# Kernel tuning notes

Hardware: AMD Instinct MI355X
Metric: run time of the kernel (lower is better)

Reference implementation:

```python
import jax, jax.numpy as jnp
import numpy as np

D_MODEL = 1024
N_HEADS = 16
D_K = D_MODEL // N_HEADS
B, T = 4, 2048


def setup_inputs() -> dict:
    key = jax.random.key(0)
    ks = jax.random.split(key, 12)
    s = 1.0 / np.sqrt(D_MODEL)
    inp = {
        "query": jax.random.normal(ks[0], (B, T, D_MODEL), dtype=jnp.float32),
        "key": jax.random.normal(ks[1], (B, T, D_MODEL), dtype=jnp.float32),
        "value": jax.random.normal(ks[2], (B, T, D_MODEL), dtype=jnp.float32),
        # causal mask, broadcastable over batch and heads
        "mask": jnp.tril(jnp.ones((T, T), dtype=bool))[None, None, :, :],
        "W_q": jax.random.uniform(ks[3], (D_MODEL, D_MODEL), jnp.float32, -s, s),
        "b_q": jnp.zeros((D_MODEL,), jnp.float32),
        "W_k": jax.random.uniform(ks[4], (D_MODEL, D_MODEL), jnp.float32, -s, s),
        "b_k": jnp.zeros((D_MODEL,), jnp.float32),
        "W_v": jax.random.uniform(ks[5], (D_MODEL, D_MODEL), jnp.float32, -s, s),
        "b_v": jnp.zeros((D_MODEL,), jnp.float32),
        "W_o": jax.random.uniform(ks[6], (D_MODEL, D_MODEL), jnp.float32, -s, s),
        "b_o": jnp.zeros((D_MODEL,), jnp.float32),
    }
    return inp


def _split_heads(x):
    b, t, _ = x.shape
    return x.reshape(b, t, N_HEADS, D_K).transpose(0, 2, 1, 3)  # [B,H,T,Dk]


def reference(query, key, value, mask, W_q, b_q, W_k, b_k, W_v, b_v, W_o, b_o):
    q = _split_heads(query @ W_q.T + b_q)
    k = _split_heads(key @ W_k.T + b_k)
    v = _split_heads(value @ W_v.T + b_v)
    scale = 1.0 / jnp.sqrt(jnp.asarray(D_K, q.dtype))
    scores = jnp.einsum("bhqd,bhkd->bhqk", q, k) * scale  # [B,H,Tq,Tk]
    scores = jnp.where(mask, scores, jnp.asarray(-jnp.inf, scores.dtype))
    attn = jax.nn.softmax(scores, axis=-1)
    out = jnp.einsum("bhqk,bhkd->bhqd", attn, v)
    out = out.transpose(0, 2, 1, 3).reshape(query.shape[0], query.shape[1], D_MODEL)
    return out @ W_o.T + b_o
```

## Files before the change

### kernel.cpp

```cpp
#include <hip/hip_runtime.h>
#include <stdint.h>
#include <stddef.h>


typedef __attribute__((ext_vector_type(4))) float f32x4;
typedef __attribute__((ext_vector_type(8))) _Float16 f16x8;
typedef __attribute__((ext_vector_type(4))) _Float16 f16x4;

#define DEV __device__ __forceinline__

constexpr int BATCH = 4, SEQ = 2048, NH = 16, DK = 64, DM = 1024;
constexpr int MROWS = BATCH * SEQ;
constexpr float QSCALE = 0.125f * 1.4426950408889634f;

DEV void async16(const void* g, void* l) {
  __builtin_amdgcn_global_load_lds(
      (const __attribute__((address_space(1))) unsigned int*)g,
      (__attribute__((address_space(3))) unsigned int*)l, 16, 0, 0);
}

__global__ void cvt_w_kernel(const float* __restrict__ w0, const float* __restrict__ w1,
                             const float* __restrict__ w2, const float* __restrict__ w3,
                             _Float16* __restrict__ o0, _Float16* __restrict__ o1,
                             _Float16* __restrict__ o2, _Float16* __restrict__ o3) {
  size_t i = (size_t)blockIdx.x * blockDim.x + threadIdx.x;
  const float* ws[4] = {w0, w1, w2, w3};
  _Float16* os[4] = {o0, o1, o2, o3};
#pragma unroll
  for (int m = 0; m < 4; m++) {
    f32x4 x = *(const f32x4*)(ws[m] + i * 4);
    f16x4 h;
#pragma unroll
    for (int j = 0; j < 4; j++) h[j] = (_Float16)x[j];
    *(f16x4*)(os[m] + i * 4) = h;
  }
}

__global__ void cvt_act_kernel(const float* __restrict__ a0, const float* __restrict__ a1,
                               const float* __restrict__ a2, _Float16* __restrict__ o0,
                               _Float16* __restrict__ o1, _Float16* __restrict__ o2) {
  size_t i = (size_t)blockIdx.x * blockDim.x + threadIdx.x;
  const float* as[3] = {a0, a1, a2};
  _Float16* os[3] = {o0, o1, o2};
#pragma unroll
  for (int m = 0; m < 3; m++) {
    f32x4 x = *(const f32x4*)(as[m] + i * 4);
    f16x4 h;
#pragma unroll
    for (int j = 0; j < 4; j++) h[j] = (_Float16)x[j];
    *(f16x4*)(os[m] + i * 4) = h;
  }
}

struct QKVPtrs {
  const float* a32[3];
  const _Float16* a16[3];
  const _Float16* w[3];
  const float* bias[3];
  _Float16* out[3];
};

template <bool AH>
__global__ __launch_bounds__(256) void gemm_qkv_kernel(QKVPtrs P) {
  constexpr int K = DM;
  __shared__ __align__(16) _Float16 smem[128 * 144];
  _Float16* As = smem;
  _Float16* Bs = smem + 8192;
  const int z = blockIdx.z;
  const _Float16* Bw = P.w[z];
  const int tid = threadIdx.x;
  const int wave = tid >> 6, lane = tid & 63;
  const int quad = lane >> 4, l16 = lane & 15;
  const int wm = wave >> 1, wn = wave & 1;
  const int m0 = blockIdx.x * 128, n0 = blockIdx.y * 128;
  const float scale = (z == 0) ? QSCALE : 1.0f;

  const f32x4 zero4 = {0.f, 0.f, 0.f, 0.f};
  f32x4 acc[4][4];
#pragma unroll
  for (int mt = 0; mt < 4; mt++)
#pragma unroll
    for (int nt = 0; nt < 4; nt++) acc[mt][nt] = zero4;

  float bv[4];
#pragma unroll
  for (int nt = 0; nt < 4; nt++) bv[nt] = P.bias[z][n0 + wn * 64 + nt * 16 + l16];

  for (int kt = 0; kt < K / 64; kt++) {
    const int k0 = kt * 64;
#pragma unroll
    for (int it = 0; it < 4; it++) {
      int idx = it * 256 + tid;
      async16(Bw + (size_t)(n0 + (idx >> 3)) * K + k0 + (idx & 7) * 8,
              (char*)Bs + (size_t)(it * 256 + wave * 64) * 16);
    }
    if (AH) {
      const _Float16* Af = P.a16[z];
#pragma unroll
      for (int it = 0; it < 4; it++) {
        int idx = it * 256 + tid;
        async16(Af + (size_t)(m0 + (idx >> 3)) * K + k0 + (idx & 7) * 8,
                (char*)As + (size_t)(it * 256 + wave * 64) * 16);
      }
    } else {
      const float* Af = P.a32[z];
#pragma unroll
      for (int it = 0; it < 4; it++) {
        int idx = it * 256 + tid;
        int row = idx >> 3, seg = idx & 7;
        const float* g = Af + (size_t)(m0 + row) * K + k0 + seg * 8;
        f32x4 x0 = *(const f32x4*)g;
        f32x4 x1 = *(const f32x4*)(g + 4);
        f16x8 h;
#pragma unroll
        for (int j = 0; j < 4; j++) { h[j] = (_Float16)x0[j]; h[4 + j] = (_Float16)x1[j]; }
        *(f16x8*)&As[row * 64 + seg * 8] = h;
      }
    }
    __syncthreads();
#pragma unroll
    for (int ks = 0; ks < 2; ks++) {
      f16x8 af[4], bfr[4];
#pragma unroll
      for (int mt = 0; mt < 4; mt++)
        af[mt] = *(const f16x8*)&As[(wm * 64 + mt * 16 + l16) * 64 + ks * 32 + quad * 8];
#pragma unroll
      for (int nt = 0; nt < 4; nt++)
        bfr[nt] = *(const f16x8*)&Bs[(wn * 64 + nt * 16 + l16) * 64 + ks * 32 + quad * 8];
#pragma unroll
      for (int mt = 0; mt < 4; mt++)
#pragma unroll
        for (int nt = 0; nt < 4; nt++)
          acc[mt][nt] = __builtin_amdgcn_mfma_f32_16x16x32_f16(af[mt], bfr[nt], acc[mt][nt], 0, 0, 0);
    }
    __syncthreads();
  }

  _Float16* Ct = smem;
  const int b = m0 >> 11, tbase = m0 & (SEQ - 1);
  if (z < 2) {
#pragma unroll
    for (int mt = 0; mt < 4; mt++)
#pragma unroll
      for (int nt = 0; nt < 4; nt++)
#pragma unroll
        for (int i = 0; i < 4; i++)
          Ct[(wm * 64 + mt * 16 + quad * 4 + i) * 144 + wn * 64 + nt * 16 + l16] =
              (_Float16)((acc[mt][nt][i] + bv[nt]) * scale);
  } else {
#pragma unroll
    for (int mt = 0; mt < 4; mt++)
#pragma unroll
      for (int nt = 0; nt < 4; nt++)
#pragma unroll
        for (int i = 0; i < 4; i++)
          Ct[(wn * 64 + nt * 16 + l16) * 144 + wm * 64 + mt * 16 + quad * 4 + i] =
              (_Float16)(acc[mt][nt][i] + bv[nt]);
  }
  __syncthreads();
  _Float16* out = P.out[z];
  if (z < 2) {
    const int row = tid >> 1, coff = (tid & 1) * 32;
#pragma unroll
    for (int hh = 0; hh < 2; hh++) {
      int h = (n0 >> 6) + hh;
      size_t gb = ((size_t)(b * NH + h) * SEQ + tbase) * 64 + (size_t)tid * 32;
#pragma unroll
      for (int k2 = 0; k2 < 4; k2++)
        *(f16x8*)&out[gb + k2 * 8] =
            *(const f16x8*)&Ct[row * 144 + hh * 64 + coff + k2 * 8];
    }
  } else {
#pragma unroll
    for (int k2 = 0; k2 < 8; k2++) {
      int c = k2 * 256 + tid;
      int n = c >> 4, s2 = c & 15;
      int h = (n0 + n) >> 6, d = (n0 + n) & (DK - 1);
      size_t gb = ((size_t)(b * NH + h) * DK + d) * SEQ + tbase + s2 * 8;
      *(f16x8*)&out[gb] = *(const f16x8*)&Ct[n * 144 + s2 * 8];
    }
  }
}

__global__ __launch_bounds__(256) void gemm_out_kernel(
    const _Float16* __restrict__ Ah, const _Float16* __restrict__ Bw,
    const float* __restrict__ bias, float* __restrict__ Cp) {
  constexpr int K = DM;
  __shared__ __align__(16) _Float16 As[128 * 64];
  __shared__ __align__(16) _Float16 Bs[128 * 64];
  const int tid = threadIdx.x;
  const int wave = tid >> 6, lane = tid & 63;
  const int quad = lane >> 4, l16 = lane & 15;
  const int wm = wave >> 1, wn = wave & 1;
  const int m0 = blockIdx.x * 128, n0 = blockIdx.y * 128;

  const f32x4 zero4 = {0.f, 0.f, 0.f, 0.f};
  f32x4 acc[4][4];
#pragma unroll
  for (int mt = 0; mt < 4; mt++)
#pragma unroll
    for (int nt = 0; nt < 4; nt++) acc[mt][nt] = zero4;

  float bv[4];
#pragma unroll
  for (int nt = 0; nt < 4; nt++) bv[nt] = bias[n0 + wn * 64 + nt * 16 + l16];

  for (int kt = 0; kt < K / 64; kt++) {
    const int k0 = kt * 64;
#pragma unroll
    for (int it = 0; it < 4; it++) {
      int idx = it * 256 + tid;
      async16(Bw + (size_t)(n0 + (idx >> 3)) * K + k0 + (idx & 7) * 8,
              (char*)Bs + (size_t)(it * 256 + wave * 64) * 16);
    }
#pragma unroll
    for (int it = 0; it < 4; it++) {
      int idx = it * 256 + tid;
      async16(Ah + (size_t)(m0 + (idx >> 3)) * K + k0 + (idx & 7) * 8,
              (char*)As + (size_t)(it * 256 + wave * 64) * 16);
    }
    __syncthreads();
#pragma unroll
    for (int ks = 0; ks < 2; ks++) {
      f16x8 af[4], bfr[4];
#pragma unroll
      for (int mt = 0; mt < 4; mt++)
        af[mt] = *(const f16x8*)&As[(wm * 64 + mt * 16 + l16) * 64 + ks * 32 + quad * 8];
#pragma unroll
      for (int nt = 0; nt < 4; nt++)
        bfr[nt] = *(const f16x8*)&Bs[(wn * 64 + nt * 16 + l16) * 64 + ks * 32 + quad * 8];
#pragma unroll
      for (int mt = 0; mt < 4; mt++)
#pragma unroll
        for (int nt = 0; nt < 4; nt++)
          acc[mt][nt] = __builtin_amdgcn_mfma_f32_16x16x32_f16(af[mt], bfr[nt], acc[mt][nt], 0, 0, 0);
    }
    __syncthreads();
  }
#pragma unroll
  for (int mt = 0; mt < 4; mt++)
#pragma unroll
    for (int nt = 0; nt < 4; nt++)
#pragma unroll
      for (int i = 0; i < 4; i++) {
        int m = m0 + wm * 64 + mt * 16 + quad * 4 + i;
        int n = n0 + wn * 64 + nt * 16 + l16;
        Cp[(size_t)m * DM + n] = acc[mt][nt][i] + bv[nt];
      }
}

__global__ __launch_bounds__(256, 2) void attn_kernel(
    const _Float16* __restrict__ Q, const _Float16* __restrict__ Kt,
    const _Float16* __restrict__ V, _Float16* __restrict__ O) {
  __shared__ __align__(16) _Float16 Ks[128 * 72];
  __shared__ __align__(16) _Float16 Vs[64 * 136];
  const int tid = threadIdx.x;
  const int wave = tid >> 6, lane = tid & 63, quad = lane >> 4, l16 = lane & 15;
  const int bh = blockIdx.y;
  const size_t base = (size_t)bh * SEQ * DK;
  const int b = bh >> 4, h = bh & 15;
  const f32x4 zero4 = {0.f, 0.f, 0.f, 0.f};

  for (int p = 0; p < 2; p++) {
    const int qt = (p == 0) ? (int)blockIdx.x : 15 - (int)blockIdx.x;
    const int t0 = qt * 128;

    f16x8 qf[2][2];
#pragma unroll
    for (int mt = 0; mt < 2; mt++)
#pragma unroll
      for (int ks = 0; ks < 2; ks++)
        qf[mt][ks] = *(const f16x8*)(Q + base + (size_t)(t0 + wave * 32 + mt * 16 + l16) * DK +
                                     ks * 32 + quad * 8);

    f32x4 oacc[2][4];
#pragma unroll
    for (int mt = 0; mt < 2; mt++)
#pragma unroll
      for (int nt = 0; nt < 4; nt++) oacc[mt][nt] = zero4;
    float mrow[2] = {-1e30f, -1e30f}, lrow[2] = {0.f, 0.f};

    for (int j = 0; j <= qt; j++) {
#pragma unroll
      for (int it = 0; it < 4; it++) {
        int c = it * 256 + tid;
        int row = c >> 3, off = (c & 7) * 8;
        *(f16x8*)&Ks[row * 72 + off] =
            *(const f16x8*)(Kt + base + (size_t)(j * 128 + row) * 64 + off);
      }
#pragma unroll
      for (int it = 0; it < 4; it++) {
        int c = it * 256 + tid;
        int d = c >> 4, off = (c & 15) * 8;
        *(f16x8*)&Vs[d * 136 + off] =
            *(const f16x8*)(V + base + ((size_t)d << 11) + j * 128 + off);
      }
      __syncthreads();

      f32x4 s[2][8];
#pragma unroll
      for (int nt = 0; nt < 8; nt++) {
        f16x8 kf0 = *(const f16x8*)&Ks[(nt * 16 + l16) * 72 + quad * 8];
        f16x8 kf1 = *(const f16x8*)&Ks[(nt * 16 + l16) * 72 + 32 + quad * 8];
#pragma unroll
        for (int mt = 0; mt < 2; mt++) {
          f32x4 zz = zero4;
          zz = __builtin_amdgcn_mfma_f32_16x16x32_f16(kf0, qf[mt][0], zz, 0, 0, 0);
          zz = __builtin_amdgcn_mfma_f32_16x16x32_f16(kf1, qf[mt][1], zz, 0, 0, 0);
          s[mt][nt] = zz;
        }
      }
      if (j == qt) {
#pragma unroll
        for (int mt = 0; mt < 2; mt++) {
          int qloc = wave * 32 + mt * 16 + l16;
#pragma unroll
          for (int nt = 0; nt < 8; nt++)
#pragma unroll
            for (int i = 0; i < 4; i++)
              if (nt * 16 + quad * 4 + i > qloc) s[mt][nt][i] = -1e30f;
        }
      }
#pragma unroll
      for (int mt = 0; mt < 2; mt++) {
        float mx = mrow[mt];
#pragma unroll
        for (int nt = 0; nt < 8; nt++)
#pragma unroll
          for (int i = 0; i < 4; i++) mx = fmaxf(mx, s[mt][nt][i]);
        mx = fmaxf(mx, __shfl_xor(mx, 16));
        mx = fmaxf(mx, __shfl_xor(mx, 32));
        float alpha = __builtin_exp2f(mrow[mt] - mx);
        mrow[mt] = mx;
        float rs = 0.f;
#pragma unroll
        for (int nt = 0; nt < 8; nt++)
#pragma unroll
          for (int i = 0; i < 4; i++) {
            float pv = __builtin_exp2f(s[mt][nt][i] - mx);
            s[mt][nt][i] = pv;
            rs += pv;
          }
        rs += __shfl_xor(rs, 16);
        rs += __shfl_xor(rs, 32);
        lrow[mt] = lrow[mt] * alpha + rs;
#pragma unroll
        for (int i = 0; i < 4; i++) {
          float ab = __shfl(alpha, quad * 4 + i);
#pragma unroll
          for (int nt = 0; nt < 4; nt++) oacc[mt][nt][i] *= ab;
        }
      }
#pragma unroll
      for (int jj = 0; jj < 8; jj++) {
        f16x4 pf[2];
#pragma unroll
        for (int mt = 0; mt < 2; mt++) {
          f16x4 t;
#pragma unroll
          for (int i = 0; i < 4; i++) t[i] = (_Float16)s[mt][jj][i];
          pf[mt] = t;
        }
#pragma unroll
        for (int nt = 0; nt < 4; nt++) {
          f16x4 vb = *(const f16x4*)&Vs[(nt * 16 + l16) * 136 + jj * 16 + quad * 4];
#pragma unroll
          for (int mt = 0; mt < 2; mt++)
            oacc[mt][nt] = __builtin_amdgcn_mfma_f32_16x16x16f16(pf[mt], vb, oacc[mt][nt], 0, 0, 0);
        }
      }
      __syncthreads();
    }
#pragma unroll
    for (int mt = 0; mt < 2; mt++) {
      float linv = 1.0f / lrow[mt];
#pragma unroll
      for (int i = 0; i < 4; i++) {
        float lb = __shfl(linv, quad * 4 + i);
        int t = t0 + wave * 32 + mt * 16 + quad * 4 + i;
#pragma unroll
        for (int nt = 0; nt < 4; nt++) {
          int d = nt * 16 + l16;
          O[((size_t)(b * SEQ + t) << 10) + h * 64 + d] = (_Float16)(oacc[mt][nt][i] * lb);
        }
      }
    }
  }
}

extern "C" void kernel_launch(void* const* d_in, const int* in_sizes, int n_in,
                              void* d_out, int out_size, void* d_ws, size_t ws_size,
                              hipStream_t stream) {
  const float* query = (const float*)d_in[0];
  const float* key_  = (const float*)d_in[1];
  const float* value = (const float*)d_in[2];
  const float* W_q = (const float*)d_in[4];
  const float* b_q = (const float*)d_in[5];
  const float* W_k = (const float*)d_in[6];
  const float* b_k = (const float*)d_in[7];
  const float* W_v = (const float*)d_in[8];
  const float* b_v = (const float*)d_in[9];
  const float* W_o = (const float*)d_in[10];
  const float* b_o = (const float*)d_in[11];

  constexpr size_t WEL = (size_t)DM * DM;
  constexpr size_t MEL = (size_t)MROWS * DM;
  _Float16* ws = (_Float16*)d_ws;
  _Float16* wq = ws;
  _Float16* wk = wq + WEL;
  _Float16* wv = wk + WEL;
  _Float16* wo = wv + WEL;

  const bool big = ws_size >= (size_t)(4 * WEL + 6 * MEL) * sizeof(_Float16);

  QKVPtrs P;
  P.a32[0] = query; P.a32[1] = key_; P.a32[2] = value;
  P.w[0] = wq; P.w[1] = wk; P.w[2] = wv;
  P.bias[0] = b_q; P.bias[1] = b_k; P.bias[2] = b_v;

  cvt_w_kernel<<<dim3((unsigned)(WEL / 4 / 256)), 256, 0, stream>>>(
      W_q, W_k, W_v, W_o, wq, wk, wv, wo);

  _Float16 *qb, *kb, *vb, *ab;
  if (big) {
    _Float16* qh = wo + WEL;
    _Float16* kh = qh + MEL;
    _Float16* vh = kh + MEL;
    qb = vh + MEL; kb = qb + MEL; vb = kb + MEL;
    ab = qh;
    P.a16[0] = qh; P.a16[1] = kh; P.a16[2] = vh;
    P.out[0] = qb; P.out[1] = kb; P.out[2] = vb;
    cvt_act_kernel<<<dim3((unsigned)(MEL / 4 / 256)), 256, 0, stream>>>(
        query, key_, value, qh, kh, vh);
    gemm_qkv_kernel<true><<<dim3(MROWS / 128, DM / 128, 3), 256, 0, stream>>>(P);
  } else {
    qb = wo + WEL; kb = qb + MEL; vb = kb + MEL; ab = vb + MEL;
    P.a16[0] = P.a16[1] = P.a16[2] = nullptr;
    P.out[0] = qb; P.out[1] = kb; P.out[2] = vb;
    gemm_qkv_kernel<false><<<dim3(MROWS / 128, DM / 128, 3), 256, 0, stream>>>(P);
  }

  attn_kernel<<<dim3(8, BATCH * NH), 256, 0, stream>>>(qb, kb, vb, ab);

  gemm_out_kernel<<<dim3(MROWS / 128, DM / 128), 256, 0, stream>>>(ab, wo, b_o, (float*)d_out);
}
```

Baseline: 364.4 us.

## Double-buffer K/V tiles in attention and fuse activation conversion into QKV GEMM

The attention kernel now prefetches the next K/V tile into registers while computing on the current one. It uses two LDS buffers so one barrier per iteration is dropped. The separate fp32-to-fp16 activation conversion pass is removed and the QKV GEMM always converts on the fly, which cuts an extra read/write pass over the activations but loses the async LDS load path for A. The attention grid is transposed so blocks for the same head launch adjacently, and the occupancy hint of 2 is dropped. Doubled LDS usage may reduce occupancy.

New measurement: 397.3 us. +9.0%, slower.

```diff
diff --git a/kernel.cpp b/kernel.cpp
--- a/kernel.cpp
+++ b/kernel.cpp
@@ -36,31 +36,13 @@
   }
 }
 
-__global__ void cvt_act_kernel(const float* __restrict__ a0, const float* __restrict__ a1,
-                               const float* __restrict__ a2, _Float16* __restrict__ o0,
-                               _Float16* __restrict__ o1, _Float16* __restrict__ o2) {
-  size_t i = (size_t)blockIdx.x * blockDim.x + threadIdx.x;
-  const float* as[3] = {a0, a1, a2};
-  _Float16* os[3] = {o0, o1, o2};
-#pragma unroll
-  for (int m = 0; m < 3; m++) {
-    f32x4 x = *(const f32x4*)(as[m] + i * 4);
-    f16x4 h;
-#pragma unroll
-    for (int j = 0; j < 4; j++) h[j] = (_Float16)x[j];
-    *(f16x4*)(os[m] + i * 4) = h;
-  }
-}
-
 struct QKVPtrs {
   const float* a32[3];
-  const _Float16* a16[3];
   const _Float16* w[3];
   const float* bias[3];
   _Float16* out[3];
 };
 
-template <bool AH>
 __global__ __launch_bounds__(256) void gemm_qkv_kernel(QKVPtrs P) {
   constexpr int K = DM;
   __shared__ __align__(16) _Float16 smem[128 * 144];
@@ -68,6 +50,7 @@
   _Float16* Bs = smem + 8192;
   const int z = blockIdx.z;
   const _Float16* Bw = P.w[z];
+  const float* Af = P.a32[z];
   const int tid = threadIdx.x;
   const int wave = tid >> 6, lane = tid & 63;
   const int quad = lane >> 4, l16 = lane & 15;
@@ -94,28 +77,17 @@
       async16(Bw + (size_t)(n0 + (idx >> 3)) * K + k0 + (idx & 7) * 8,
               (char*)Bs + (size_t)(it * 256 + wave * 64) * 16);
     }
-    if (AH) {
-      const _Float16* Af = P.a16[z];
-#pragma unroll
-      for (int it = 0; it < 4; it++) {
-        int idx = it * 256 + tid;
-        async16(Af + (size_t)(m0 + (idx >> 3)) * K + k0 + (idx & 7) * 8,
-                (char*)As + (size_t)(it * 256 + wave * 64) * 16);
-      }
-    } else {
-      const float* Af = P.a32[z];
-#pragma unroll
-      for (int it = 0; it < 4; it++) {
-        int idx = it * 256 + tid;
-        int row = idx >> 3, seg = idx & 7;
-        const float* g = Af + (size_t)(m0 + row) * K + k0 + seg * 8;
-        f32x4 x0 = *(const f32x4*)g;
-        f32x4 x1 = *(const f32x4*)(g + 4);
-        f16x8 h;
-#pragma unroll
-        for (int j = 0; j < 4; j++) { h[j] = (_Float16)x0[j]; h[4 + j] = (_Float16)x1[j]; }
-        *(f16x8*)&As[row * 64 + seg * 8] = h;
-      }
+#pragma unroll
+    for (int it = 0; it < 4; it++) {
+      int idx = it * 256 + tid;
+      int row = idx >> 3, seg = idx & 7;
+      const float* g = Af + (size_t)(m0 + row) * K + k0 + seg * 8;
+      f32x4 x0 = *(const f32x4*)g;
+      f32x4 x1 = *(const f32x4*)(g + 4);
+      f16x8 h;
+#pragma unroll
+      for (int j = 0; j < 4; j++) { h[j] = (_Float16)x0[j]; h[4 + j] = (_Float16)x1[j]; }
+      *(f16x8*)&As[row * 64 + seg * 8] = h;
     }
     __syncthreads();
 #pragma unroll
@@ -249,20 +221,23 @@
       }
 }
 
-__global__ __launch_bounds__(256, 2) void attn_kernel(
+__global__ __launch_bounds__(256) void attn_kernel(
     const _Float16* __restrict__ Q, const _Float16* __restrict__ Kt,
     const _Float16* __restrict__ V, _Float16* __restrict__ O) {
-  __shared__ __align__(16) _Float16 Ks[128 * 72];
-  __shared__ __align__(16) _Float16 Vs[64 * 136];
+  __shared__ __align__(16) _Float16 Ks[2][128 * 72];
+  __shared__ __align__(16) _Float16 Vs[2][64 * 136];
   const int tid = threadIdx.x;
   const int wave = tid >> 6, lane = tid & 63, quad = lane >> 4, l16 = lane & 15;
-  const int bh = blockIdx.y;
+  const int bh = blockIdx.x, xp = blockIdx.y;
   const size_t base = (size_t)bh * SEQ * DK;
   const int b = bh >> 4, h = bh & 15;
   const f32x4 zero4 = {0.f, 0.f, 0.f, 0.f};
 
+  const int ck_row = tid >> 3, ck_off = (tid & 7) * 8;
+  const int cv_d = tid >> 4, cv_off = (tid & 15) * 8;
+
   for (int p = 0; p < 2; p++) {
-    const int qt = (p == 0) ? (int)blockIdx.x : 15 - (int)blockIdx.x;
+    const int qt = (p == 0) ? xp : 15 - xp;
     const int t0 = qt * 128;
 
     f16x8 qf[2][2];
@@ -273,6 +248,14 @@
         qf[mt][ks] = *(const f16x8*)(Q + base + (size_t)(t0 + wave * 32 + mt * 16 + l16) * DK +
                                      ks * 32 + quad * 8);
 
+    f16x8 kreg[4], vreg[4];
+#pragma unroll
+    for (int it = 0; it < 4; it++)
+      kreg[it] = *(const f16x8*)(Kt + base + (size_t)(it * 32 + ck_row) * 64 + ck_off);
+#pragma unroll
+    for (int it = 0; it < 4; it++)
+      vreg[it] = *(const f16x8*)(V + base + ((size_t)(it * 16 + cv_d) << 11) + cv_off);
+
     f32x4 oacc[2][4];
 #pragma unroll
     for (int mt = 0; mt < 2; mt++)
@@ -281,27 +264,29 @@
     float mrow[2] = {-1e30f, -1e30f}, lrow[2] = {0.f, 0.f};
 
     for (int j = 0; j <= qt; j++) {
-#pragma unroll
-      for (int it = 0; it < 4; it++) {
-        int c = it * 256 + tid;
-        int row = c >> 3, off = (c & 7) * 8;
-        *(f16x8*)&Ks[row * 72 + off] =
-            *(const f16x8*)(Kt + base + (size_t)(j * 128 + row) * 64 + off);
-      }
-#pragma unroll
-      for (int it = 0; it < 4; it++) {
-        int c = it * 256 + tid;
-        int d = c >> 4, off = (c & 15) * 8;
-        *(f16x8*)&Vs[d * 136 + off] =
-            *(const f16x8*)(V + base + ((size_t)d << 11) + j * 128 + off);
-      }
+      const int buf = j & 1;
+      _Float16* ksb = Ks[buf];
+      _Float16* vsb = Vs[buf];
+#pragma unroll
+      for (int it = 0; it < 4; it++)
+        *(f16x8*)&ksb[(it * 32 + ck_row) * 72 + ck_off] = kreg[it];
+#pragma unroll
+      for (int it = 0; it < 4; it++)
+        *(f16x8*)&vsb[(it * 16 + cv_d) * 136 + cv_off] = vreg[it];
       __syncthreads();
+      const int jn = (j < qt) ? j + 1 : qt;
+#pragma unroll
+      for (int it = 0; it < 4; it++)
+        kreg[it] = *(const f16x8*)(Kt + base + (size_t)(jn * 128 + it * 32 + ck_row) * 64 + ck_off);
+#pragma unroll
+      for (int it = 0; it < 4; it++)
+        vreg[it] = *(const f16x8*)(V + base + ((size_t)(it * 16 + cv_d) << 11) + jn * 128 + cv_off);
 
       f32x4 s[2][8];
 #pragma unroll
       for (int nt = 0; nt < 8; nt++) {
-        f16x8 kf0 = *(const f16x8*)&Ks[(nt * 16 + l16) * 72 + quad * 8];
-        f16x8 kf1 = *(const f16x8*)&Ks[(nt * 16 + l16) * 72 + 32 + quad * 8];
+        f16x8 kf0 = *(const f16x8*)&ksb[(nt * 16 + l16) * 72 + quad * 8];
+        f16x8 kf1 = *(const f16x8*)&ksb[(nt * 16 + l16) * 72 + 32 + quad * 8];
 #pragma unroll
         for (int mt = 0; mt < 2; mt++) {
           f32x4 zz = zero4;
@@ -363,13 +348,12 @@
         }
 #pragma unroll
         for (int nt = 0; nt < 4; nt++) {
-          f16x4 vb = *(const f16x4*)&Vs[(nt * 16 + l16) * 136 + jj * 16 + quad * 4];
+          f16x4 vb = *(const f16x4*)&vsb[(nt * 16 + l16) * 136 + jj * 16 + quad * 4];
 #pragma unroll
           for (int mt = 0; mt < 2; mt++)
             oacc[mt][nt] = __builtin_amdgcn_mfma_f32_16x16x16f16(pf[mt], vb, oacc[mt][nt], 0, 0, 0);
         }
       }
-      __syncthreads();
     }
 #pragma unroll
     for (int mt = 0; mt < 2; mt++) {
@@ -385,6 +369,7 @@
         }
       }
     }
+    __syncthreads();
   }
 }
 
@@ -410,37 +395,22 @@
   _Float16* wk = wq + WEL;
   _Float16* wv = wk + WEL;
   _Float16* wo = wv + WEL;
-
-  const bool big = ws_size >= (size_t)(4 * WEL + 6 * MEL) * sizeof(_Float16);
+  _Float16* qb = wo + WEL;
+  _Float16* kb = qb + MEL;
+  _Float16* vb = kb + MEL;
+  _Float16* ab = vb + MEL;
+
+  cvt_w_kernel<<<dim3((unsigned)(WEL / 4 / 256)), 256, 0, stream>>>(
+      W_q, W_k, W_v, W_o, wq, wk, wv, wo);
 
   QKVPtrs P;
   P.a32[0] = query; P.a32[1] = key_; P.a32[2] = value;
   P.w[0] = wq; P.w[1] = wk; P.w[2] = wv;
   P.bias[0] = b_q; P.bias[1] = b_k; P.bias[2] = b_v;
-
-  cvt_w_kernel<<<dim3((unsigned)(WEL / 4 / 256)), 256, 0, stream>>>(
-      W_q, W_k, W_v, W_o, wq, wk, wv, wo);
-
-  _Float16 *qb, *kb, *vb, *ab;
-  if (big) {
-    _Float16* qh = wo + WEL;
-    _Float16* kh = qh + MEL;
-    _Float16* vh = kh + MEL;
-    qb = vh + MEL; kb = qb + MEL; vb = kb + MEL;
-    ab = qh;
-    P.a16[0] = qh; P.a16[1] = kh; P.a16[2] = vh;
-    P.out[0] = qb; P.out[1] = kb; P.out[2] = vb;
-    cvt_act_kernel<<<dim3((unsigned)(MEL / 4 / 256)), 256, 0, stream>>>(
-        query, key_, value, qh, kh, vh);
-    gemm_qkv_kernel<true><<<dim3(MROWS / 128, DM / 128, 3), 256, 0, stream>>>(P);
-  } else {
-    qb = wo + WEL; kb = qb + MEL; vb = kb + MEL; ab = vb + MEL;
-    P.a16[0] = P.a16[1] = P.a16[2] = nullptr;
-    P.out[0] = qb; P.out[1] = kb; P.out[2] = vb;
-    gemm_qkv_kernel<false><<<dim3(MROWS / 128, DM / 128, 3), 256, 0, stream>>>(P);
-  }
-
-  attn_kernel<<<dim3(8, BATCH * NH), 256, 0, stream>>>(qb, kb, vb, ab);
+  P.out[0] = qb; P.out[1] = kb; P.out[2] = vb;
+  gemm_qkv_kernel<<<dim3(MROWS / 128, DM / 128, 3), 256, 0, stream>>>(P);
+
+  attn_kernel<<<dim3(BATCH * NH, 8), 256, 0, stream>>>(qb, kb, vb, ab);
 
   gemm_out_kernel<<<dim3(MROWS / 128, DM / 128), 256, 0, stream>>>(ab, wo, b_o, (float*)d_out);
 }
```
